# Kernel tuning notes

Measured on AMD Instinct MI355X. Metric: run time of the kernel, lower is better.

## Reference

```python
import jax, jax.numpy as jnp
import numpy as np

N_NODES = 50000
N_EDGES = 600000
D_IN = 128
HID = 128
N_SAGE = 2          # num_layers - 1
N_GRAPHS = 512
BN_EPS = 1e-5


def setup_inputs() -> dict:
    key = jax.random.key(0)
    ks = jax.random.split(key, 12)
    s = 1.0 / np.sqrt(HID)
    x = jax.random.normal(ks[0], (N_NODES, D_IN), dtype=jnp.float32)
    edge_index = jax.random.randint(ks[1], (2, N_EDGES), 0, N_NODES, dtype=jnp.int32)
    batch = jnp.sort(jax.random.randint(ks[2], (N_NODES,), 0, N_GRAPHS, dtype=jnp.int32))
    # GIN MLP: Linear(D_IN,HID) -> ReLU -> Linear(HID,HID)
    gin_w1 = jax.random.normal(ks[3], (D_IN, HID), dtype=jnp.float32) * s
    gin_b1 = jnp.zeros((HID,), jnp.float32)
    gin_w2 = jax.random.normal(ks[4], (HID, HID), dtype=jnp.float32) * s
    gin_b2 = jnp.zeros((HID,), jnp.float32)
    # SAGEConv layers: lin_l (neighbors, with bias), lin_r (root, no bias)
    sage_wl = jax.random.normal(ks[5], (N_SAGE, HID, HID), dtype=jnp.float32) * s
    sage_bl = jnp.zeros((N_SAGE, HID), jnp.float32)
    sage_wr = jax.random.normal(ks[6], (N_SAGE, HID, HID), dtype=jnp.float32) * s
    # BatchNorm per layer (3 layers)
    bn_gamma = jnp.ones((1 + N_SAGE, HID), jnp.float32)
    bn_beta = jnp.zeros((1 + N_SAGE, HID), jnp.float32)
    return {"x": x, "edge_index": edge_index, "batch": batch,
            "gin_w1": gin_w1, "gin_b1": gin_b1, "gin_w2": gin_w2, "gin_b2": gin_b2,
            "sage_wl": sage_wl, "sage_bl": sage_bl, "sage_wr": sage_wr,
            "bn_gamma": bn_gamma, "bn_beta": bn_beta}


def _batchnorm(h, gamma, beta):
    # training-mode BN over the node dimension (biased variance, as torch)
    mu = jnp.mean(h, axis=0)
    var = jnp.var(h, axis=0)
    return gamma * (h - mu) * jax.lax.rsqrt(var + BN_EPS) + beta


def reference(x, edge_index, batch, gin_w1, gin_b1, gin_w2, gin_b2,
              sage_wl, sage_bl, sage_wr, bn_gamma, bn_beta):
    n = x.shape[0]
    src, dst = edge_index[0], edge_index[1]

    # ---- Layer 0: GINConv (eps=0): mlp(x + sum_{j->i} x_j) ----
    agg = jax.ops.segment_sum(x[src], dst, num_segments=n)  # [N, D_IN]
    h = x + agg
    h = jax.nn.relu(h @ gin_w1 + gin_b1) @ gin_w2 + gin_b2
    h = jax.nn.relu(_batchnorm(h, bn_gamma[0], bn_beta[0]))
    # dropout is identity (eval mode)

    # degree for mean aggregation (shared across SAGE layers)
    deg = jax.ops.segment_sum(jnp.ones((src.shape[0],), h.dtype), dst, num_segments=n)
    inv_deg = (1.0 / jnp.maximum(deg, 1.0))[:, None]  # [N,1]

    # ---- SAGE layers: lin_l(mean_{j->i} h_j) + lin_r(h_i) ----
    for l in range(N_SAGE):
        neigh = jax.ops.segment_sum(h[src], dst, num_segments=n) * inv_deg
        h = neigh @ sage_wl[l] + sage_bl[l] + h @ sage_wr[l]
        h = jax.nn.relu(_batchnorm(h, bn_gamma[l + 1], bn_beta[l + 1]))

    # ---- global mean pool over batch ids ----
    sums = jax.ops.segment_sum(h, batch, num_segments=N_GRAPHS)  # [G, HID]
    counts = jax.ops.segment_sum(jnp.ones((n,), h.dtype), batch, num_segments=N_GRAPHS)
    return sums / jnp.maximum(counts, 1.0)[:, None]
```

## Files before the change

kernel.cpp:

```cpp
#include <hip/hip_runtime.h>

#define N_NODES 50000
#define N_EDGES 600000
#define HID 128
#define N_GRAPHS 512
#define BN_EPS 1e-5f
#define INV_N (1.0f / 50000.0f)

typedef __attribute__((ext_vector_type(8))) short bf16x8;
typedef __attribute__((ext_vector_type(4))) float f32x4;

__device__ __forceinline__ unsigned short f2b(float f) {
    unsigned u = __float_as_uint(f);
    return (unsigned short)((u + 0x7FFFu + ((u >> 16) & 1u)) >> 16);
}
__device__ __forceinline__ float b2f(unsigned short h) {
    return __uint_as_float(((unsigned)h) << 16);
}

#define CONVX_BLOCKS 6250
#define WCONV_BLOCKS 384
#define DEG_BLOCKS   2344
__global__ __launch_bounds__(256) void prep_kernel(
    const float* __restrict__ x, const float* __restrict__ gw1, const float* __restrict__ gw2,
    const float* __restrict__ swl, const float* __restrict__ swr, const int* __restrict__ dst,
    unsigned short* __restrict__ x16, unsigned short* __restrict__ wt, int* __restrict__ deg)
{
    int b = blockIdx.x;
    int t = threadIdx.x;
    if (b < CONVX_BLOCKS) {
        int gid = b * 256 + t;
        int i = gid >> 5, l = gid & 31;
        if (i >= N_NODES) return;
        int c0 = l * 4;
        float4 v = *(const float4*)(x + (size_t)i * 128 + c0);
        ushort4 o;
        o.x = f2b(v.x); o.y = f2b(v.y); o.z = f2b(v.z); o.w = f2b(v.w);
        *(ushort4*)(x16 + (size_t)i * 128 + c0) = o;
    } else if (b < CONVX_BLOCKS + WCONV_BLOCKS) {
        int gid = (b - CONVX_BLOCKS) * 256 + t;
        int m = gid >> 14;
        int e = gid & 16383;
        int k = e >> 7;
        int n = e & 127;
        const float* src = (m == 0) ? gw1 : (m == 1) ? gw2 : (m == 2) ? swl
                         : (m == 3) ? swr : (m == 4) ? (swl + 16384) : (swr + 16384);
        wt[m * 16384 + n * 128 + k] = f2b(src[k * 128 + n]);
    } else {
        int e = (b - CONVX_BLOCKS - WCONV_BLOCKS) * 256 + t;
        if (e < N_EDGES) atomicAdd(&deg[dst[e]], 1);
    }
}

#define ALLOC_BLOCKS 196
__global__ __launch_bounds__(256) void alloc_kernel(int* __restrict__ cursor,
                                                    int* __restrict__ row_beg,
                                                    float* __restrict__ inv_deg,
                                                    int* __restrict__ total,
                                                    const int* __restrict__ batch,
                                                    int* __restrict__ gstart) {
    if (blockIdx.x >= ALLOC_BLOCKS) {
        int g = (blockIdx.x - ALLOC_BLOCKS) * 256 + threadIdx.x;
        if (g > N_GRAPHS) return;
        int lo = 0, hi = N_NODES;
        while (lo < hi) {
            int mid = (lo + hi) >> 1;
            if (batch[mid] < g) lo = mid + 1; else hi = mid;
        }
        gstart[g] = lo;
        return;
    }
    __shared__ int tmp[256];
    __shared__ int base;
    int i = blockIdx.x * 256 + threadIdx.x;
    int d = (i < N_NODES) ? cursor[i] : 0;
    tmp[threadIdx.x] = d;
    __syncthreads();
#pragma unroll
    for (int off = 1; off < 256; off <<= 1) {
        int v = (threadIdx.x >= off) ? tmp[threadIdx.x - off] : 0;
        __syncthreads();
        tmp[threadIdx.x] += v;
        __syncthreads();
    }
    if (threadIdx.x == 255) base = atomicAdd(total, tmp[255]);
    __syncthreads();
    if (i < N_NODES) {
        int b = base + tmp[threadIdx.x] - d;
        row_beg[i] = b;
        cursor[i] = b;
        inv_deg[i] = 1.0f / fmaxf((float)d, 1.0f);
    }
}

__global__ void csr_fill_kernel(const int* __restrict__ src, const int* __restrict__ dst,
                                int* __restrict__ cursor, int* __restrict__ csr_src, int nE) {
    int e = blockIdx.x * blockDim.x + threadIdx.x;
    if (e < nE) {
        int pos = atomicAdd(&cursor[dst[e]], 1);
        csr_src[pos] = src[e];
    }
}

template<bool AFF, bool MEAN, bool HACT>
__global__ __launch_bounds__(256) void aggregate_kernel(
    const unsigned short* __restrict__ feat,
    const int* __restrict__ row_beg, const int* __restrict__ row_end,
    const int* __restrict__ csr_src,
    const float* __restrict__ stats, const float* __restrict__ gamma,
    const float* __restrict__ beta, const float* __restrict__ inv_deg,
    unsigned short* __restrict__ agg, unsigned short* __restrict__ hact, int n)
{
    int gid = blockIdx.x * blockDim.x + threadIdx.x;
    int node = gid >> 4;
    int lane = gid & 15;
    if (node >= n) return;
    int c0 = lane * 8;

    float cc[8], ss[8];
    if (AFF) {
#pragma unroll
        for (int j = 0; j < 8; j++) {
            int col = c0 + j;
            float mu = stats[col] * INV_N;
            float var = stats[128 + col] * INV_N - mu * mu;
            float rs = rsqrtf(var + BN_EPS);
            float c = gamma[col] * rs;
            cc[j] = c;
            ss[j] = beta[col] - mu * c;
        }
    }

    float a[8];
#pragma unroll
    for (int j = 0; j < 8; j++) a[j] = 0.f;

    int beg = row_beg[node];
    int end = row_end[node];
    int e = beg;
    for (; e + 3 < end; e += 4) {
        int s0 = csr_src[e];
        int s1 = csr_src[e + 1];
        int s2 = csr_src[e + 2];
        int s3 = csr_src[e + 3];
        bf16x8 v0 = *(const bf16x8*)(feat + (size_t)s0 * 128 + c0);
        bf16x8 v1 = *(const bf16x8*)(feat + (size_t)s1 * 128 + c0);
        bf16x8 v2 = *(const bf16x8*)(feat + (size_t)s2 * 128 + c0);
        bf16x8 v3 = *(const bf16x8*)(feat + (size_t)s3 * 128 + c0);
#pragma unroll
        for (int j = 0; j < 8; j++) {
            float t0 = b2f((unsigned short)v0[j]);
            float t1 = b2f((unsigned short)v1[j]);
            float t2 = b2f((unsigned short)v2[j]);
            float t3 = b2f((unsigned short)v3[j]);
            if (AFF) {
                t0 = fmaxf(t0 * cc[j] + ss[j], 0.f);
                t1 = fmaxf(t1 * cc[j] + ss[j], 0.f);
                t2 = fmaxf(t2 * cc[j] + ss[j], 0.f);
                t3 = fmaxf(t3 * cc[j] + ss[j], 0.f);
            }
            a[j] += (t0 + t1) + (t2 + t3);
        }
    }
    for (; e < end; e++) {
        int s0 = csr_src[e];
        bf16x8 v0 = *(const bf16x8*)(feat + (size_t)s0 * 128 + c0);
#pragma unroll
        for (int j = 0; j < 8; j++) {
            float t0 = b2f((unsigned short)v0[j]);
            if (AFF) t0 = fmaxf(t0 * cc[j] + ss[j], 0.f);
            a[j] += t0;
        }
    }

    if (MEAN) {
        float s = inv_deg[node];
#pragma unroll
        for (int j = 0; j < 8; j++) a[j] *= s;
    }
    bf16x8 o;
#pragma unroll
    for (int j = 0; j < 8; j++) o[j] = (short)f2b(a[j]);
    *(bf16x8*)(agg + (size_t)node * 128 + c0) = o;

    if (HACT) {
        bf16x8 v = *(const bf16x8*)(feat + (size_t)node * 128 + c0);
        bf16x8 h;
#pragma unroll
        for (int j = 0; j < 8; j++)
            h[j] = (short)f2b(fmaxf(b2f((unsigned short)v[j]) * cc[j] + ss[j], 0.f));
        *(bf16x8*)(hact + (size_t)node * 128 + c0) = h;
    }
}

__global__ __launch_bounds__(256, 2) void gemm_gin_kernel(
    const unsigned short* __restrict__ X, const unsigned short* __restrict__ AGG,
    const unsigned short* __restrict__ W1t, const unsigned short* __restrict__ W2t,
    const float* __restrict__ b1, const float* __restrict__ b2,
    float* __restrict__ stats, unsigned short* __restrict__ Cb,
    int M, int ntiles)
{
    __shared__ unsigned short t1[32][136];
    __shared__ float red[2][128];

    const int t = threadIdx.x;
    const int wave = t >> 6;
    const int lane = t & 63;
    const int colhalf = wave & 1;
    const int rowpair = wave >> 1;
    const int m16 = lane & 15;
    const int quad = lane >> 4;
    const int k0 = quad * 8;
    const int colbase = colhalf * 64;
    const int lrow = rowpair * 16 + m16;

    const bf16x8 zero8 = {0, 0, 0, 0, 0, 0, 0, 0};

    bf16x8 w1f[4][4], w2f[4][4];
#pragma unroll
    for (int ct = 0; ct < 4; ct++) {
        int col = colbase + ct * 16 + m16;
#pragma unroll
        for (int kc = 0; kc < 4; kc++) {
            w1f[ct][kc] = *(const bf16x8*)(W1t + (size_t)col * 128 + kc * 32 + k0);
            w2f[ct][kc] = *(const bf16x8*)(W2t + (size_t)col * 128 + kc * 32 + k0);
        }
    }
    f32x4 bs1[4], bs2[4];
#pragma unroll
    for (int ct = 0; ct < 4; ct++) {
        bs1[ct] = *(const f32x4*)(b1 + colbase + ct * 16 + quad * 4);
        bs2[ct] = *(const f32x4*)(b2 + colbase + ct * 16 + quad * 4);
    }

    float psum[4][4], psq[4][4];
#pragma unroll
    for (int ct = 0; ct < 4; ct++)
#pragma unroll
        for (int r = 0; r < 4; r++) { psum[ct][r] = 0.f; psq[ct][r] = 0.f; }

    for (int tile = blockIdx.x; tile < ntiles; tile += gridDim.x) {
        int arow = tile * 32 + rowpair * 16 + m16;
        bool aok = arow < M;

        bf16x8 a[4];
#pragma unroll
        for (int kc = 0; kc < 4; kc++) {
            if (aok) {
                bf16x8 vx = *(const bf16x8*)(X + (size_t)arow * 128 + kc * 32 + k0);
                bf16x8 vg = *(const bf16x8*)(AGG + (size_t)arow * 128 + kc * 32 + k0);
                bf16x8 r;
#pragma unroll
                for (int i = 0; i < 8; i++)
                    r[i] = (short)f2b(b2f((unsigned short)vx[i]) + b2f((unsigned short)vg[i]));
                a[kc] = r;
            } else {
                a[kc] = zero8;
            }
        }

        f32x4 acc[4];
#pragma unroll
        for (int ct = 0; ct < 4; ct++) acc[ct] = (f32x4){0.f, 0.f, 0.f, 0.f};
#pragma unroll
        for (int kc = 0; kc < 4; kc++)
#pragma unroll
            for (int ct = 0; ct < 4; ct++)
                acc[ct] = __builtin_amdgcn_mfma_f32_16x16x32_bf16(w1f[ct][kc], a[kc], acc[ct], 0, 0, 0);

        __syncthreads();
#pragma unroll
        for (int ct = 0; ct < 4; ct++) {
            f32x4 v = acc[ct] + bs1[ct];
            ushort4 o;
            o.x = f2b(fmaxf(v[0], 0.f));
            o.y = f2b(fmaxf(v[1], 0.f));
            o.z = f2b(fmaxf(v[2], 0.f));
            o.w = f2b(fmaxf(v[3], 0.f));
            *(ushort4*)&t1[lrow][colbase + ct * 16 + quad * 4] = o;
        }
        __syncthreads();

        bf16x8 ta[4];
#pragma unroll
        for (int kc = 0; kc < 4; kc++)
            ta[kc] = *(const bf16x8*)&t1[lrow][kc * 32 + k0];

        f32x4 acc2[4];
#pragma unroll
        for (int ct = 0; ct < 4; ct++) acc2[ct] = (f32x4){0.f, 0.f, 0.f, 0.f};
#pragma unroll
        for (int kc = 0; kc < 4; kc++)
#pragma unroll
            for (int ct = 0; ct < 4; ct++)
                acc2[ct] = __builtin_amdgcn_mfma_f32_16x16x32_bf16(w2f[ct][kc], ta[kc], acc2[ct], 0, 0, 0);

        int orow = arow;
        if (orow < M) {
#pragma unroll
            for (int ct = 0; ct < 4; ct++) {
                f32x4 v = acc2[ct] + bs2[ct];
                int col = colbase + ct * 16 + quad * 4;
#pragma unroll
                for (int r = 0; r < 4; r++) { psum[ct][r] += v[r]; psq[ct][r] += v[r] * v[r]; }
                ushort4 o;
                o.x = f2b(v[0]); o.y = f2b(v[1]); o.z = f2b(v[2]); o.w = f2b(v[3]);
                *(ushort4*)(Cb + (size_t)orow * 128 + col) = o;
            }
        }
    }

#pragma unroll
    for (int ct = 0; ct < 4; ct++)
#pragma unroll
        for (int r = 0; r < 4; r++) {
#pragma unroll
            for (int mask = 1; mask <= 8; mask <<= 1) {
                psum[ct][r] += __shfl_xor(psum[ct][r], mask, 64);
                psq[ct][r]  += __shfl_xor(psq[ct][r], mask, 64);
            }
        }
    __syncthreads();
    if (m16 == 0) {
#pragma unroll
        for (int ct = 0; ct < 4; ct++)
#pragma unroll
            for (int r = 0; r < 4; r++)
                red[rowpair][colbase + ct * 16 + quad * 4 + r] = psum[ct][r];
    }
    __syncthreads();
    if (t < 128) atomicAdd(&stats[t], red[0][t] + red[1][t]);
    __syncthreads();
    if (m16 == 0) {
#pragma unroll
        for (int ct = 0; ct < 4; ct++)
#pragma unroll
            for (int r = 0; r < 4; r++)
                red[rowpair][colbase + ct * 16 + quad * 4 + r] = psq[ct][r];
    }
    __syncthreads();
    if (t < 128) atomicAdd(&stats[128 + t], red[0][t] + red[1][t]);
}

__global__ __launch_bounds__(256) void gemm_dual_kernel(
    const unsigned short* __restrict__ A1, const unsigned short* __restrict__ A2,
    const unsigned short* __restrict__ W1t, const unsigned short* __restrict__ W2t,
    const float* __restrict__ bias, float* __restrict__ stats,
    unsigned short* __restrict__ Cb, int M, int ntiles)
{
    __shared__ float red[128];

    const int t = threadIdx.x;
    const int wave = t >> 6;
    const int lane = t & 63;
    const int m16 = lane & 15;
    const int quad = lane >> 4;
    const int k0 = quad * 8;
    const int colbase = wave * 32;

    const bf16x8 zero8 = {0, 0, 0, 0, 0, 0, 0, 0};

    bf16x8 w1f[2][4], w2f[2][4];
#pragma unroll
    for (int ct = 0; ct < 2; ct++) {
        int col = colbase + ct * 16 + m16;
#pragma unroll
        for (int kc = 0; kc < 4; kc++) {
            w1f[ct][kc] = *(const bf16x8*)(W1t + (size_t)col * 128 + kc * 32 + k0);
            w2f[ct][kc] = *(const bf16x8*)(W2t + (size_t)col * 128 + kc * 32 + k0);
        }
    }
    f32x4 bs[2];
#pragma unroll
    for (int ct = 0; ct < 2; ct++)
        bs[ct] = *(const f32x4*)(bias + colbase + ct * 16 + quad * 4);

    float psum[2][4], psq[2][4];
#pragma unroll
    for (int ct = 0; ct < 2; ct++)
#pragma unroll
        for (int r = 0; r < 4; r++) { psum[ct][r] = 0.f; psq[ct][r] = 0.f; }

    bf16x8 a1[4], a2[4], a1n[4], a2n[4];

    int tile = blockIdx.x;
    if (tile < ntiles) {
        int arow = tile * 16 + m16;
        bool aok = arow < M;
#pragma unroll
        for (int kc = 0; kc < 4; kc++) {
            a1[kc] = aok ? *(const bf16x8*)(A1 + (size_t)arow * 128 + kc * 32 + k0) : zero8;
            a2[kc] = aok ? *(const bf16x8*)(A2 + (size_t)arow * 128 + kc * 32 + k0) : zero8;
        }
    }

    for (; tile < ntiles; tile += gridDim.x) {
        int nt = tile + gridDim.x;
        if (nt < ntiles) {
            int arow = nt * 16 + m16;
            bool aok = arow < M;
#pragma unroll
            for (int kc = 0; kc < 4; kc++) {
                a1n[kc] = aok ? *(const bf16x8*)(A1 + (size_t)arow * 128 + kc * 32 + k0) : zero8;
                a2n[kc] = aok ? *(const bf16x8*)(A2 + (size_t)arow * 128 + kc * 32 + k0) : zero8;
            }
        }

        f32x4 acc[2];
        acc[0] = (f32x4){0.f, 0.f, 0.f, 0.f};
        acc[1] = (f32x4){0.f, 0.f, 0.f, 0.f};
#pragma unroll
        for (int kc = 0; kc < 4; kc++) {
#pragma unroll
            for (int ct = 0; ct < 2; ct++) {
                acc[ct] = __builtin_amdgcn_mfma_f32_16x16x32_bf16(w1f[ct][kc], a1[kc], acc[ct], 0, 0, 0);
                acc[ct] = __builtin_amdgcn_mfma_f32_16x16x32_bf16(w2f[ct][kc], a2[kc], acc[ct], 0, 0, 0);
            }
        }

        int orow = tile * 16 + m16;
        if (orow < M) {
#pragma unroll
            for (int ct = 0; ct < 2; ct++) {
                f32x4 v = acc[ct] + bs[ct];
                int col = colbase + ct * 16 + quad * 4;
#pragma unroll
                for (int r = 0; r < 4; r++) { psum[ct][r] += v[r]; psq[ct][r] += v[r] * v[r]; }
                ushort4 o;
                o.x = f2b(v[0]); o.y = f2b(v[1]); o.z = f2b(v[2]); o.w = f2b(v[3]);
                *(ushort4*)(Cb + (size_t)orow * 128 + col) = o;
            }
        }

        if (nt < ntiles) {
            a1[0] = a1n[0]; a1[1] = a1n[1]; a1[2] = a1n[2]; a1[3] = a1n[3];
            a2[0] = a2n[0]; a2[1] = a2n[1]; a2[2] = a2n[2]; a2[3] = a2n[3];
        }
    }

#pragma unroll
    for (int ct = 0; ct < 2; ct++)
#pragma unroll
        for (int r = 0; r < 4; r++) {
#pragma unroll
            for (int mask = 1; mask <= 8; mask <<= 1) {
                psum[ct][r] += __shfl_xor(psum[ct][r], mask, 64);
                psq[ct][r]  += __shfl_xor(psq[ct][r], mask, 64);
            }
        }
    if (m16 == 0) {
#pragma unroll
        for (int ct = 0; ct < 2; ct++)
#pragma unroll
            for (int r = 0; r < 4; r++)
                red[colbase + ct * 16 + quad * 4 + r] = psum[ct][r];
    }
    __syncthreads();
    if (t < 128) atomicAdd(&stats[t], red[t]);
    __syncthreads();
    if (m16 == 0) {
#pragma unroll
        for (int ct = 0; ct < 2; ct++)
#pragma unroll
            for (int r = 0; r < 4; r++)
                red[colbase + ct * 16 + quad * 4 + r] = psq[ct][r];
    }
    __syncthreads();
    if (t < 128) atomicAdd(&stats[128 + t], red[t]);
}

__global__ __launch_bounds__(128) void pool_mean_kernel(const unsigned short* __restrict__ h,
                                                        const int* __restrict__ gstart,
                                                        const float* __restrict__ stats,
                                                        const float* __restrict__ gamma,
                                                        const float* __restrict__ beta,
                                                        float* __restrict__ out) {
    int g = blockIdx.x;
    int col = threadIdx.x;
    float mu = stats[col] * INV_N;
    float var = stats[128 + col] * INV_N - mu * mu;
    float rs = rsqrtf(var + BN_EPS);
    float c = gamma[col] * rs;
    float b = beta[col] - mu * c;
    int beg = gstart[g];
    int end = gstart[g + 1];
    float s = 0.f;
    int i = beg;
    for (; i + 1 < end; i += 2) {
        float v0 = b2f(h[(size_t)i * 128 + col]);
        float v1 = b2f(h[(size_t)(i + 1) * 128 + col]);
        s += fmaxf(v0 * c + b, 0.f) + fmaxf(v1 * c + b, 0.f);
    }
    if (i < end)
        s += fmaxf(b2f(h[(size_t)i * 128 + col]) * c + b, 0.f);
    float cnt = fmaxf((float)(end - beg), 1.0f);
    out[(size_t)g * 128 + col] = s / cnt;
}

extern "C" void kernel_launch(void* const* d_in, const int* in_sizes, int n_in,
                              void* d_out, int out_size, void* d_ws, size_t ws_size,
                              hipStream_t stream) {
    const float* x    = (const float*)d_in[0];
    const int*   ei   = (const int*)d_in[1];
    const int*   src  = ei;
    const int*   dst  = ei + N_EDGES;
    const int*   batch = (const int*)d_in[2];
    const float* gw1  = (const float*)d_in[3];
    const float* gb1  = (const float*)d_in[4];
    const float* gw2  = (const float*)d_in[5];
    const float* gb2  = (const float*)d_in[6];
    const float* swl  = (const float*)d_in[7];
    const float* sbl  = (const float*)d_in[8];
    const float* swr  = (const float*)d_in[9];
    const float* bng  = (const float*)d_in[10];
    const float* bnb  = (const float*)d_in[11];
    float* out = (float*)d_out;

    float* ws = (float*)d_ws;
    unsigned short* x16    = (unsigned short*)(ws + 0);
    unsigned short* agg16  = (unsigned short*)(ws + 3200000);
    unsigned short* hact16 = (unsigned short*)(ws + 6400000);
    unsigned short* hpre16 = (unsigned short*)(ws + 9600000);
    unsigned short* wt     = (unsigned short*)(ws + 12800000);
    float*          inv_deg= ws + 12850000;
    int*            row_beg= (int*)(ws + 12900000);
    int*            cursor = (int*)(ws + 12950000);
    int*            total  = cursor + 50000;
    float*          stats  = (float*)(cursor + 50001);
    int*            csr_src= (int*)(ws + 13100000);
    int*            gstart = (int*)(ws + 13700000);

    const int aggr_blocks = (N_NODES * 16 + 255) / 256;
    const int ntiles32 = (N_NODES + 31) / 32;
    const int ntiles16 = (N_NODES + 15) / 16;
    const int ggrid = 512;

    hipMemsetAsync(cursor, 0, (50001 + 768) * sizeof(int), stream);

    prep_kernel<<<CONVX_BLOCKS + WCONV_BLOCKS + DEG_BLOCKS, 256, 0, stream>>>(
        x, gw1, gw2, swl, swr, dst, x16, wt, cursor);

    alloc_kernel<<<ALLOC_BLOCKS + 3, 256, 0, stream>>>(cursor, row_beg, inv_deg, total, batch, gstart);
    csr_fill_kernel<<<(N_EDGES + 255) / 256, 256, 0, stream>>>(src, dst, cursor, csr_src, N_EDGES);

    aggregate_kernel<false, false, false><<<aggr_blocks, 256, 0, stream>>>(
        x16, row_beg, cursor, csr_src, nullptr, nullptr, nullptr, nullptr, agg16, nullptr, N_NODES);
    gemm_gin_kernel<<<ggrid, 256, 0, stream>>>(
        x16, agg16, wt + 0 * 16384, wt + 1 * 16384, gb1, gb2, stats + 0, hpre16, N_NODES, ntiles32);

    aggregate_kernel<true, true, true><<<aggr_blocks, 256, 0, stream>>>(
        hpre16, row_beg, cursor, csr_src, stats + 0, bng + 0 * HID, bnb + 0 * HID, inv_deg,
        agg16, hact16, N_NODES);
    gemm_dual_kernel<<<ggrid, 256, 0, stream>>>(
        agg16, hact16, wt + 2 * 16384, wt + 3 * 16384, sbl + 0 * HID, stats + 256, hpre16, N_NODES, ntiles16);

    aggregate_kernel<true, true, true><<<aggr_blocks, 256, 0, stream>>>(
        hpre16, row_beg, cursor, csr_src, stats + 256, bng + 1 * HID, bnb + 1 * HID, inv_deg,
        agg16, hact16, N_NODES);
    gemm_dual_kernel<<<ggrid, 256, 0, stream>>>(
        agg16, hact16, wt + 4 * 16384, wt + 5 * 16384, sbl + 1 * HID, stats + 512, hpre16, N_NODES, ntiles16);

    pool_mean_kernel<<<N_GRAPHS, 128, 0, stream>>>(
        hpre16, gstart, stats + 512, bng + 2 * HID, bnb + 2 * HID, out);
}
```

Measured before the change: 363.1 us.

## Stage 16-bit CSR indices in LDS, unroll gathers, vectorize mean pool

```diff
diff --git a/kernel.cpp b/kernel.cpp
--- a/kernel.cpp
+++ b/kernel.cpp
@@ -94,28 +94,40 @@
 }
 
 __global__ void csr_fill_kernel(const int* __restrict__ src, const int* __restrict__ dst,
-                                int* __restrict__ cursor, int* __restrict__ csr_src, int nE) {
+                                int* __restrict__ cursor, unsigned short* __restrict__ csr_src, int nE) {
     int e = blockIdx.x * blockDim.x + threadIdx.x;
     if (e < nE) {
         int pos = atomicAdd(&cursor[dst[e]], 1);
-        csr_src[pos] = src[e];
-    }
-}
-
+        csr_src[pos] = (unsigned short)src[e];
+    }
+}
+
+#define IDXCAP 2048
 template<bool AFF, bool MEAN, bool HACT>
 __global__ __launch_bounds__(256) void aggregate_kernel(
     const unsigned short* __restrict__ feat,
     const int* __restrict__ row_beg, const int* __restrict__ row_end,
-    const int* __restrict__ csr_src,
+    const unsigned short* __restrict__ csr_src,
     const float* __restrict__ stats, const float* __restrict__ gamma,
     const float* __restrict__ beta, const float* __restrict__ inv_deg,
     unsigned short* __restrict__ agg, unsigned short* __restrict__ hact, int n)
 {
-    int gid = blockIdx.x * blockDim.x + threadIdx.x;
-    int node = gid >> 4;
-    int lane = gid & 15;
+    __shared__ unsigned short idxbuf[IDXCAP];
+    const int t = threadIdx.x;
+    const int node0 = blockIdx.x * 16;
+    const int node = node0 + (t >> 4);
+    const int lane = t & 15;
+    const int c0 = lane * 8;
+
+    const int last = (node0 + 15 < n) ? node0 + 15 : n - 1;
+    const int ebeg = row_beg[node0];
+    const int ecnt = row_end[last] - ebeg;
+    const bool lds_ok = (ecnt <= IDXCAP);
+    if (lds_ok) {
+        for (int i = t; i < ecnt; i += 256) idxbuf[i] = csr_src[ebeg + i];
+    }
+    __syncthreads();
     if (node >= n) return;
-    int c0 = lane * 8;
 
     float cc[8], ss[8];
     if (AFF) {
@@ -135,41 +147,93 @@
 #pragma unroll
     for (int j = 0; j < 8; j++) a[j] = 0.f;
 
-    int beg = row_beg[node];
-    int end = row_end[node];
-    int e = beg;
-    for (; e + 3 < end; e += 4) {
-        int s0 = csr_src[e];
-        int s1 = csr_src[e + 1];
-        int s2 = csr_src[e + 2];
-        int s3 = csr_src[e + 3];
-        bf16x8 v0 = *(const bf16x8*)(feat + (size_t)s0 * 128 + c0);
-        bf16x8 v1 = *(const bf16x8*)(feat + (size_t)s1 * 128 + c0);
-        bf16x8 v2 = *(const bf16x8*)(feat + (size_t)s2 * 128 + c0);
-        bf16x8 v3 = *(const bf16x8*)(feat + (size_t)s3 * 128 + c0);
-#pragma unroll
-        for (int j = 0; j < 8; j++) {
-            float t0 = b2f((unsigned short)v0[j]);
-            float t1 = b2f((unsigned short)v1[j]);
-            float t2 = b2f((unsigned short)v2[j]);
-            float t3 = b2f((unsigned short)v3[j]);
-            if (AFF) {
-                t0 = fmaxf(t0 * cc[j] + ss[j], 0.f);
-                t1 = fmaxf(t1 * cc[j] + ss[j], 0.f);
-                t2 = fmaxf(t2 * cc[j] + ss[j], 0.f);
-                t3 = fmaxf(t3 * cc[j] + ss[j], 0.f);
-            }
-            a[j] += (t0 + t1) + (t2 + t3);
-        }
-    }
-    for (; e < end; e++) {
-        int s0 = csr_src[e];
-        bf16x8 v0 = *(const bf16x8*)(feat + (size_t)s0 * 128 + c0);
-#pragma unroll
-        for (int j = 0; j < 8; j++) {
-            float t0 = b2f((unsigned short)v0[j]);
-            if (AFF) t0 = fmaxf(t0 * cc[j] + ss[j], 0.f);
-            a[j] += t0;
+    const int beg = row_beg[node];
+    const int deg = row_end[node] - beg;
+
+    if (lds_ok) {
+        const int off = beg - ebeg;
+        int e = 0;
+        for (; e + 7 < deg; e += 8) {
+            int s[8];
+#pragma unroll
+            for (int u = 0; u < 8; u++) s[u] = idxbuf[off + e + u];
+            bf16x8 v[8];
+#pragma unroll
+            for (int u = 0; u < 8; u++)
+                v[u] = *(const bf16x8*)(feat + (size_t)s[u] * 128 + c0);
+#pragma unroll
+            for (int u = 0; u < 8; u++) {
+#pragma unroll
+                for (int j = 0; j < 8; j++) {
+                    float tv = b2f((unsigned short)v[u][j]);
+                    if (AFF) tv = fmaxf(tv * cc[j] + ss[j], 0.f);
+                    a[j] += tv;
+                }
+            }
+        }
+        for (; e + 3 < deg; e += 4) {
+            int s[4];
+#pragma unroll
+            for (int u = 0; u < 4; u++) s[u] = idxbuf[off + e + u];
+            bf16x8 v[4];
+#pragma unroll
+            for (int u = 0; u < 4; u++)
+                v[u] = *(const bf16x8*)(feat + (size_t)s[u] * 128 + c0);
+#pragma unroll
+            for (int u = 0; u < 4; u++) {
+#pragma unroll
+                for (int j = 0; j < 8; j++) {
+                    float tv = b2f((unsigned short)v[u][j]);
+                    if (AFF) tv = fmaxf(tv * cc[j] + ss[j], 0.f);
+                    a[j] += tv;
+                }
+            }
+        }
+        for (; e < deg; e++) {
+            int s0 = idxbuf[off + e];
+            bf16x8 v0 = *(const bf16x8*)(feat + (size_t)s0 * 128 + c0);
+#pragma unroll
+            for (int j = 0; j < 8; j++) {
+                float tv = b2f((unsigned short)v0[j]);
+                if (AFF) tv = fmaxf(tv * cc[j] + ss[j], 0.f);
+                a[j] += tv;
+            }
+        }
+    } else {
+        int e = beg, end = beg + deg;
+        for (; e + 3 < end; e += 4) {
+            int s0 = csr_src[e];
+            int s1 = csr_src[e + 1];
+            int s2 = csr_src[e + 2];
+            int s3 = csr_src[e + 3];
+            bf16x8 v0 = *(const bf16x8*)(feat + (size_t)s0 * 128 + c0);
+            bf16x8 v1 = *(const bf16x8*)(feat + (size_t)s1 * 128 + c0);
+            bf16x8 v2 = *(const bf16x8*)(feat + (size_t)s2 * 128 + c0);
+            bf16x8 v3 = *(const bf16x8*)(feat + (size_t)s3 * 128 + c0);
+#pragma unroll
+            for (int j = 0; j < 8; j++) {
+                float t0 = b2f((unsigned short)v0[j]);
+                float t1 = b2f((unsigned short)v1[j]);
+                float t2 = b2f((unsigned short)v2[j]);
+                float t3 = b2f((unsigned short)v3[j]);
+                if (AFF) {
+                    t0 = fmaxf(t0 * cc[j] + ss[j], 0.f);
+                    t1 = fmaxf(t1 * cc[j] + ss[j], 0.f);
+                    t2 = fmaxf(t2 * cc[j] + ss[j], 0.f);
+                    t3 = fmaxf(t3 * cc[j] + ss[j], 0.f);
+                }
+                a[j] += (t0 + t1) + (t2 + t3);
+            }
+        }
+        for (; e < end; e++) {
+            int s0 = csr_src[e];
+            bf16x8 v0 = *(const bf16x8*)(feat + (size_t)s0 * 128 + c0);
+#pragma unroll
+            for (int j = 0; j < 8; j++) {
+                float t0 = b2f((unsigned short)v0[j]);
+                if (AFF) t0 = fmaxf(t0 * cc[j] + ss[j], 0.f);
+                a[j] += t0;
+            }
         }
     }
 
@@ -475,26 +539,46 @@
                                                         const float* __restrict__ gamma,
                                                         const float* __restrict__ beta,
                                                         float* __restrict__ out) {
+    __shared__ float red[8][128];
     int g = blockIdx.x;
-    int col = threadIdx.x;
-    float mu = stats[col] * INV_N;
-    float var = stats[128 + col] * INV_N - mu * mu;
-    float rs = rsqrtf(var + BN_EPS);
-    float c = gamma[col] * rs;
-    float b = beta[col] - mu * c;
+    int t = threadIdx.x;
+    int lane = t & 15, grp = t >> 4;
+    int c0 = lane * 8;
+    float c[8], b[8];
+#pragma unroll
+    for (int j = 0; j < 8; j++) {
+        int col = c0 + j;
+        float mu = stats[col] * INV_N;
+        float var = stats[128 + col] * INV_N - mu * mu;
+        float rs = rsqrtf(var + BN_EPS);
+        c[j] = gamma[col] * rs;
+        b[j] = beta[col] - mu * c[j];
+    }
     int beg = gstart[g];
     int end = gstart[g + 1];
-    float s = 0.f;
-    int i = beg;
-    for (; i + 1 < end; i += 2) {
-        float v0 = b2f(h[(size_t)i * 128 + col]);
-        float v1 = b2f(h[(size_t)(i + 1) * 128 + col]);
-        s += fmaxf(v0 * c + b, 0.f) + fmaxf(v1 * c + b, 0.f);
-    }
-    if (i < end)
-        s += fmaxf(b2f(h[(size_t)i * 128 + col]) * c + b, 0.f);
-    float cnt = fmaxf((float)(end - beg), 1.0f);
-    out[(size_t)g * 128 + col] = s / cnt;
+    float s[8];
+#pragma unroll
+    for (int j = 0; j < 8; j++) s[j] = 0.f;
+    for (int i = beg + grp; i < end; i += 8) {
+        bf16x8 v = *(const bf16x8*)(h + (size_t)i * 128 + c0);
+#pragma unroll
+        for (int j = 0; j < 8; j++)
+            s[j] += fmaxf(b2f((unsigned short)v[j]) * c[j] + b[j], 0.f);
+    }
+#pragma unroll
+    for (int j = 0; j < 8; j++) red[grp][c0 + j] = s[j];
+    __syncthreads();
+    if (t < 16) {
+        float cnt = fmaxf((float)(end - beg), 1.0f);
+        int cc0 = t * 8;
+#pragma unroll
+        for (int j = 0; j < 8; j++) {
+            float tot = 0.f;
+#pragma unroll
+            for (int r = 0; r < 8; r++) tot += red[r][cc0 + j];
+            out[(size_t)g * 128 + cc0 + j] = tot / cnt;
+        }
+    }
 }
 
 extern "C" void kernel_launch(void* const* d_in, const int* in_sizes, int n_in,
@@ -527,10 +611,10 @@
     int*            cursor = (int*)(ws + 12950000);
     int*            total  = cursor + 50000;
     float*          stats  = (float*)(cursor + 50001);
-    int*            csr_src= (int*)(ws + 13100000);
+    unsigned short* csr_src= (unsigned short*)(ws + 13100000);
     int*            gstart = (int*)(ws + 13700000);
 
-    const int aggr_blocks = (N_NODES * 16 + 255) / 256;
+    const int aggr_blocks = (N_NODES + 15) / 16;
     const int ntiles32 = (N_NODES + 31) / 32;
     const int ntiles16 = (N_NODES + 15) / 16;
     const int ggrid = 512;
```

After: 348.9 us. 1.04x faster.
